# Optimization experiments

Hardware: AMD Instinct MI355X
Metric: run time of the kernel (lower is better)

The kernel has to match this reference:

```python
import jax, jax.numpy as jnp
import numpy as np

# dims
B, S, D, H, F = 4, 1024, 1024, 16, 4096
DH = D // H
THETA0 = 1.0   # base firing threshold of AdaptiveLIFNeuron
RHO = 0.9      # adaptation decay
EPS = 1e-5


def layer_norm(x, g, b):
    mu = jnp.mean(x, axis=-1, keepdims=True)
    var = jnp.mean((x - mu) ** 2, axis=-1, keepdims=True)
    return (x - mu) * jax.lax.rsqrt(var + EPS) * g + b


def spike(u):
    # Heaviside forward, sigmoid surrogate gradient (straight-through)
    sg = jax.nn.sigmoid(4.0 * u)
    hard = (u > 0).astype(u.dtype)
    return sg + jax.lax.stop_gradient(hard - sg)


def setup_inputs() -> dict:
    key = jax.random.key(0)
    ks = jax.random.split(key, 8)
    std = 0.02
    w = lambda k, shape: jax.random.normal(k, shape, jnp.float32) * std
    return {
        "x": jax.random.normal(ks[0], (B, S, D), jnp.float32),
        "Wq": w(ks[1], (D, D)), "bq": jnp.zeros((D,), jnp.float32),
        "Wk": w(ks[2], (D, D)), "bk": jnp.zeros((D,), jnp.float32),
        "Wv": w(ks[3], (D, D)), "bv": jnp.zeros((D,), jnp.float32),
        "Wo": w(ks[4], (D, D)), "bo": jnp.zeros((D,), jnp.float32),
        "g1": jnp.ones((D,), jnp.float32), "b1": jnp.zeros((D,), jnp.float32),
        "W1": w(ks[5], (D, F)), "bf1": jnp.zeros((F,), jnp.float32),
        "W2": w(ks[6], (F, D)), "bf2": jnp.zeros((D,), jnp.float32),
        "g2": jnp.ones((D,), jnp.float32), "b2": jnp.zeros((D,), jnp.float32),
        "decay": jnp.full((F,), 0.8, jnp.float32),  # per-feature membrane leak
        "beta": jnp.full((F,), 0.1, jnp.float32),   # per-feature threshold adaptation
    }


def reference(x, Wq, bq, Wk, bk, Wv, bv, Wo, bo, g1, b1, W1, bf1, W2, bf2, g2, b2, decay, beta):
    # --- causal multi-head self-attention (DSALayer) ---
    q = (x @ Wq + bq).reshape(B, S, H, DH)
    k = (x @ Wk + bk).reshape(B, S, H, DH)
    v = (x @ Wv + bv).reshape(B, S, H, DH)
    scores = jnp.einsum("bqhd,bkhd->bhqk", q, k) / np.sqrt(DH).astype(np.float32)
    causal = jnp.tril(jnp.ones((S, S), bool))
    scores = jnp.where(causal, scores, jnp.asarray(-1e9, scores.dtype))
    p = jax.nn.softmax(scores, axis=-1)
    attn = jnp.einsum("bhqk,bkhd->bqhd", p, v).reshape(B, S, D) @ Wo + bo
    h = layer_norm(x + attn, g1, b1)

    # --- feed-forward with per-timestep adaptive LIF recurrence ---
    ff = h @ W1 + bf1                      # [B, S, F]

    def step(carry, xt):
        vm, a = carry                      # membrane potential, adaptation
        vm = decay * vm + xt
        u = vm - (THETA0 + a)
        s = spike(u)
        vm = vm * (1.0 - s)                # hard reset on spike
        a = RHO * a + beta * s
        return (vm, a), s

    init = (jnp.zeros((B, F), x.dtype), jnp.zeros((B, F), x.dtype))
    _, spikes = jax.lax.scan(step, init, jnp.swapaxes(ff, 0, 1))  # scan over time
    spikes = jnp.swapaxes(spikes, 0, 1)    # [B, S, F]

    ff_out = spikes @ W2 + bf2
    return layer_norm(h + ff_out, g2, b2)
```

## Files before the change

kernel.cpp:

```cpp
#include <hip/hip_runtime.h>
#include <hip/hip_bf16.h>
#include <stdint.h>

#define Bsz 4
#define Ssz 1024
#define Dsz 1024
#define Hsz 16
#define Fsz 4096

typedef __hip_bfloat16 bf16;
typedef __attribute__((ext_vector_type(8))) short bf16x8;
typedef __attribute__((ext_vector_type(4))) float f32x4;

typedef __attribute__((address_space(1))) const void gvoid_t;
typedef __attribute__((address_space(3))) void svoid_t;

__device__ __forceinline__ void gload16(const bf16* g, bf16* l) {
    __builtin_amdgcn_global_load_lds((gvoid_t*)g, (svoid_t*)l, 16, 0, 0);
}

__global__ __launch_bounds__(256) void split_k(const float* __restrict__ src,
                                               bf16* __restrict__ hi,
                                               bf16* __restrict__ lo) {
    const int i = (blockIdx.x * 256 + threadIdx.x) * 4;
    const float4 v = *(const float4*)(src + i);
    float vv[4] = {v.x, v.y, v.z, v.w};
    #pragma unroll
    for (int u = 0; u < 4; ++u) {
        const bf16 h = __float2bfloat16(vv[u]);
        hi[i + u] = h;
        lo[i + u] = __float2bfloat16(vv[u] - __bfloat162float(h));
    }
}

__global__ __launch_bounds__(256) void transpose_split4_k(const float* __restrict__ Wq,
                                                          const float* __restrict__ Wk,
                                                          const float* __restrict__ Wv,
                                                          const float* __restrict__ Wo,
                                                          bf16* __restrict__ qkv_hi,
                                                          bf16* __restrict__ qkv_lo,
                                                          bf16* __restrict__ wo_hi,
                                                          bf16* __restrict__ wo_lo) {
    __shared__ float tile[32][33];
    const int z = blockIdx.z;
    const float* in = (z == 0) ? Wq : (z == 1) ? Wk : (z == 2) ? Wv : Wo;
    const size_t WP = (size_t)Dsz * Dsz;
    bf16* hiT = (z < 3) ? qkv_hi + (size_t)z * WP : wo_hi;
    bf16* loT = (z < 3) ? qkv_lo + (size_t)z * WP : wo_lo;
    const int bx = blockIdx.x * 32, by = blockIdx.y * 32;
    const int tx = threadIdx.x, ty = threadIdx.y;
    #pragma unroll
    for (int i = 0; i < 32; i += 8)
        tile[ty + i][tx] = in[(size_t)(by + ty + i) * Dsz + bx + tx];
    __syncthreads();
    #pragma unroll
    for (int i = 0; i < 32; i += 8) {
        const float v = tile[tx][ty + i];
        const bf16 h = __float2bfloat16(v);
        const size_t o = (size_t)(bx + ty + i) * Dsz + by + tx;
        hiT[o] = h;
        loT[o] = __float2bfloat16(v - __bfloat162float(h));
    }
}

__global__ __launch_bounds__(256) void transpose_split_k(const float* __restrict__ in,
                                                         bf16* __restrict__ hiT,
                                                         bf16* __restrict__ loT,
                                                         int R, int C) {
    __shared__ float tile[32][33];
    const int bx = blockIdx.x * 32, by = blockIdx.y * 32;
    const int tx = threadIdx.x, ty = threadIdx.y;
    #pragma unroll
    for (int i = 0; i < 32; i += 8)
        tile[ty + i][tx] = in[(size_t)(by + ty + i) * C + bx + tx];
    __syncthreads();
    #pragma unroll
    for (int i = 0; i < 32; i += 8) {
        const float v = tile[tx][ty + i];
        const bf16 h = __float2bfloat16(v);
        const size_t o = (size_t)(bx + ty + i) * R + by + tx;
        hiT[o] = h;
        loT[o] = __float2bfloat16(v - __bfloat162float(h));
    }
}

__global__ __launch_bounds__(256) void transpose_cast_k(const float* __restrict__ in,
                                                        bf16* __restrict__ outT,
                                                        int R, int C) {
    __shared__ float tile[32][33];
    const int bx = blockIdx.x * 32, by = blockIdx.y * 32;
    const int tx = threadIdx.x, ty = threadIdx.y;
    #pragma unroll
    for (int i = 0; i < 32; i += 8)
        tile[ty + i][tx] = in[(size_t)(by + ty + i) * C + bx + tx];
    __syncthreads();
    #pragma unroll
    for (int i = 0; i < 32; i += 8)
        outT[(size_t)(bx + ty + i) * R + by + tx] = __float2bfloat16(tile[tx][ty + i]);
}

__global__ __launch_bounds__(256) void gemm3_bt(const bf16* __restrict__ Ah,
                                                const bf16* __restrict__ Al,
                                                const bf16* __restrict__ Bh,
                                                const bf16* __restrict__ Bl,
                                                const float* __restrict__ bias,
                                                float* __restrict__ Cf,
                                                int M, int N, int K) {
    __shared__ alignas(16) bf16 Ash[128 * 32];
    __shared__ alignas(16) bf16 Asl[128 * 32];
    __shared__ alignas(16) bf16 Bsh[128 * 32];
    __shared__ alignas(16) bf16 Bsl[128 * 32];
    const int t = threadIdx.x;
    const int lane = t & 63, wv = t >> 6;
    const int mw = wv >> 1, nw = wv & 1;
    const int m0 = blockIdx.y * 128, n0 = blockIdx.x * 128;
    const int z = blockIdx.z, nz = gridDim.z;
    const int Ks = K / nz, koff = z * Ks;
    const int r16 = lane & 15, q8 = (lane >> 4) * 8;
    const int arow = t >> 2, acol = (t & 3) * 8;

    const bf16* gAh = Ah + (size_t)(m0 + arow) * K + koff + acol;
    const bf16* gAl = Al + (size_t)(m0 + arow) * K + koff + acol;
    const bf16* gBh = Bh + (size_t)(n0 + arow) * K + koff + acol;
    const bf16* gBl = Bl + (size_t)(n0 + arow) * K + koff + acol;
    const size_t rK64 = (size_t)64 * K;
    bf16* lAh = Ash + wv * 512;
    bf16* lAl = Asl + wv * 512;
    bf16* lBh = Bsh + wv * 512;
    bf16* lBl = Bsl + wv * 512;

    f32x4 acc[4][4] = {};

    for (int k0 = 0; k0 < Ks; k0 += 32) {
        __syncthreads();
        gload16(gAh + k0, lAh);  gload16(gAh + k0 + rK64, lAh + 2048);
        gload16(gAl + k0, lAl);  gload16(gAl + k0 + rK64, lAl + 2048);
        gload16(gBh + k0, lBh);  gload16(gBh + k0 + rK64, lBh + 2048);
        gload16(gBl + k0, lBl);  gload16(gBl + k0 + rK64, lBl + 2048);
        __syncthreads();

        bf16x8 ah[4], al[4], bh[4], bl[4];
        #pragma unroll
        for (int rt = 0; rt < 4; ++rt) {
            const int ro = (64 * mw + 16 * rt + r16) * 32 + q8;
            ah[rt] = *(const bf16x8*)(Ash + ro);
            al[rt] = *(const bf16x8*)(Asl + ro);
        }
        #pragma unroll
        for (int ct = 0; ct < 4; ++ct) {
            const int co = (64 * nw + 16 * ct + r16) * 32 + q8;
            bh[ct] = *(const bf16x8*)(Bsh + co);
            bl[ct] = *(const bf16x8*)(Bsl + co);
        }
        #pragma unroll
        for (int rt = 0; rt < 4; ++rt)
            #pragma unroll
            for (int ct = 0; ct < 4; ++ct) {
                acc[rt][ct] = __builtin_amdgcn_mfma_f32_16x16x32_bf16(ah[rt], bh[ct], acc[rt][ct], 0, 0, 0);
                acc[rt][ct] = __builtin_amdgcn_mfma_f32_16x16x32_bf16(ah[rt], bl[ct], acc[rt][ct], 0, 0, 0);
                acc[rt][ct] = __builtin_amdgcn_mfma_f32_16x16x32_bf16(al[rt], bh[ct], acc[rt][ct], 0, 0, 0);
            }
    }

    float* Cz = Cf + (size_t)z * M * N;
    const int rowi = (lane >> 4) * 4;
    const int coli = lane & 15;
    #pragma unroll
    for (int ct = 0; ct < 4; ++ct) {
        const int col = n0 + 64 * nw + 16 * ct + coli;
        const float bv = (z == 0) ? bias[col] : 0.f;
        #pragma unroll
        for (int rt = 0; rt < 4; ++rt) {
            const int rowb = m0 + 64 * mw + 16 * rt + rowi;
            #pragma unroll
            for (int r = 0; r < 4; ++r)
                Cz[(size_t)(rowb + r) * N + col] = acc[rt][ct][r] + bv;
        }
    }
}

__global__ __launch_bounds__(256) void gemm3_qkv(const bf16* __restrict__ Ah,
                                                 const bf16* __restrict__ Al,
                                                 const bf16* __restrict__ Bh,
                                                 const bf16* __restrict__ Bl,
                                                 const float* __restrict__ bias,
                                                 bf16* __restrict__ qhi, bf16* __restrict__ qlo,
                                                 bf16* __restrict__ khi, bf16* __restrict__ klo,
                                                 bf16* __restrict__ vthi, bf16* __restrict__ vtlo) {
    const int K = Dsz;
    __shared__ alignas(16) bf16 Ash[128 * 32];
    __shared__ alignas(16) bf16 Asl[128 * 32];
    __shared__ alignas(16) bf16 Bsh[128 * 32];
    __shared__ alignas(16) bf16 Bsl[128 * 32];
    const int t = threadIdx.x;
    const int lane = t & 63, wv = t >> 6;
    const int mw = wv >> 1, nw = wv & 1;
    const int m0 = blockIdx.y * 128, n0 = blockIdx.x * 128;
    const int r16 = lane & 15, q8 = (lane >> 4) * 8;
    const int arow = t >> 2, acol = (t & 3) * 8;

    const bf16* gAh = Ah + (size_t)(m0 + arow) * K + acol;
    const bf16* gAl = Al + (size_t)(m0 + arow) * K + acol;
    const bf16* gBh = Bh + (size_t)(n0 + arow) * K + acol;
    const bf16* gBl = Bl + (size_t)(n0 + arow) * K + acol;
    const size_t rK64 = (size_t)64 * K;
    bf16* lAh = Ash + wv * 512;
    bf16* lAl = Asl + wv * 512;
    bf16* lBh = Bsh + wv * 512;
    bf16* lBl = Bsl + wv * 512;

    f32x4 acc[4][4] = {};

    for (int k0 = 0; k0 < K; k0 += 32) {
        __syncthreads();
        gload16(gAh + k0, lAh);  gload16(gAh + k0 + rK64, lAh + 2048);
        gload16(gAl + k0, lAl);  gload16(gAl + k0 + rK64, lAl + 2048);
        gload16(gBh + k0, lBh);  gload16(gBh + k0 + rK64, lBh + 2048);
        gload16(gBl + k0, lBl);  gload16(gBl + k0 + rK64, lBl + 2048);
        __syncthreads();

        bf16x8 ah[4], al[4], bh[4], bl[4];
        #pragma unroll
        for (int rt = 0; rt < 4; ++rt) {
            const int ro = (64 * mw + 16 * rt + r16) * 32 + q8;
            ah[rt] = *(const bf16x8*)(Ash + ro);
            al[rt] = *(const bf16x8*)(Asl + ro);
        }
        #pragma unroll
        for (int ct = 0; ct < 4; ++ct) {
            const int co = (64 * nw + 16 * ct + r16) * 32 + q8;
            bh[ct] = *(const bf16x8*)(Bsh + co);
            bl[ct] = *(const bf16x8*)(Bsl + co);
        }
        #pragma unroll
        for (int rt = 0; rt < 4; ++rt)
            #pragma unroll
            for (int ct = 0; ct < 4; ++ct) {
                acc[rt][ct] = __builtin_amdgcn_mfma_f32_16x16x32_bf16(ah[rt], bh[ct], acc[rt][ct], 0, 0, 0);
                acc[rt][ct] = __builtin_amdgcn_mfma_f32_16x16x32_bf16(ah[rt], bl[ct], acc[rt][ct], 0, 0, 0);
                acc[rt][ct] = __builtin_amdgcn_mfma_f32_16x16x32_bf16(al[rt], bh[ct], acc[rt][ct], 0, 0, 0);
            }
    }

    const int rowi = (lane >> 4) * 4;
    const int coli = lane & 15;
    if (n0 < 2048) {
        const float scale = (n0 < 1024) ? 0.125f : 1.0f;
        bf16* hip_ = (n0 < 1024) ? qhi : khi;
        bf16* lop_ = (n0 < 1024) ? qlo : klo;
        const int cbase = (n0 < 1024) ? n0 : (n0 - 1024);
        #pragma unroll
        for (int ct = 0; ct < 4; ++ct) {
            const int col = cbase + 64 * nw + 16 * ct + coli;
            const float bv = bias[n0 + 64 * nw + 16 * ct + coli];
            #pragma unroll
            for (int rt = 0; rt < 4; ++rt) {
                const int rowb = m0 + 64 * mw + 16 * rt + rowi;
                #pragma unroll
                for (int r = 0; r < 4; ++r) {
                    const float val = (acc[rt][ct][r] + bv) * scale;
                    const bf16 h = __float2bfloat16(val);
                    const size_t off = (size_t)(rowb + r) * Dsz + col;
                    hip_[off] = h;
                    lop_[off] = __float2bfloat16(val - __bfloat162float(h));
                }
            }
        }
    } else {
        #pragma unroll
        for (int ct = 0; ct < 4; ++ct) {
            const int col = n0 + 64 * nw + 16 * ct + coli;
            const float bv = bias[col];
            const int c2 = col - 2048;
            #pragma unroll
            for (int rt = 0; rt < 4; ++rt) {
                const int rowb = m0 + 64 * mw + 16 * rt + rowi;
                const int b = rowb >> 10, s = rowb & 1023;
                bf16 hv[4], lv[4];
                #pragma unroll
                for (int r = 0; r < 4; ++r) {
                    const float val = acc[rt][ct][r] + bv;
                    hv[r] = __float2bfloat16(val);
                    lv[r] = __float2bfloat16(val - __bfloat162float(hv[r]));
                }
                const size_t vo = (size_t)b * (16 * 64 * 1024) + (size_t)c2 * 1024 + s;
                *(uint2*)&vthi[vo] = *(const uint2*)hv;
                *(uint2*)&vtlo[vo] = *(const uint2*)lv;
            }
        }
    }
}

__global__ __launch_bounds__(256) void gemm1_bt(const bf16* __restrict__ A,
                                                const bf16* __restrict__ Bt,
                                                const float* __restrict__ bias,
                                                float* __restrict__ Cf,
                                                int M, int N, int K) {
    __shared__ alignas(16) bf16 As[128 * 32];
    __shared__ alignas(16) bf16 Bs[128 * 32];
    const int t = threadIdx.x;
    const int lane = t & 63, wv = t >> 6;
    const int mw = wv >> 1, nw = wv & 1;
    const int m0 = blockIdx.y * 128, n0 = blockIdx.x * 128;
    const int z = blockIdx.z, nz = gridDim.z;
    const int Ks = K / nz, koff = z * Ks;
    const int r16 = lane & 15, q8 = (lane >> 4) * 8;
    const int arow = t >> 2, acol = (t & 3) * 8;

    const bf16* gA = A + (size_t)(m0 + arow) * K + koff + acol;
    const bf16* gB = Bt + (size_t)(n0 + arow) * K + koff + acol;
    const size_t rK64 = (size_t)64 * K;
    bf16* lA = As + wv * 512;
    bf16* lB = Bs + wv * 512;

    f32x4 acc[4][4] = {};

    for (int k0 = 0; k0 < Ks; k0 += 32) {
        __syncthreads();
        gload16(gA + k0, lA);  gload16(gA + k0 + rK64, lA + 2048);
        gload16(gB + k0, lB);  gload16(gB + k0 + rK64, lB + 2048);
        __syncthreads();

        bf16x8 af[4], bf_[4];
        #pragma unroll
        for (int rt = 0; rt < 4; ++rt)
            af[rt] = *(const bf16x8*)(As + (64 * mw + 16 * rt + r16) * 32 + q8);
        #pragma unroll
        for (int ct = 0; ct < 4; ++ct)
            bf_[ct] = *(const bf16x8*)(Bs + (64 * nw + 16 * ct + r16) * 32 + q8);
        #pragma unroll
        for (int rt = 0; rt < 4; ++rt)
            #pragma unroll
            for (int ct = 0; ct < 4; ++ct)
                acc[rt][ct] = __builtin_amdgcn_mfma_f32_16x16x32_bf16(
                    af[rt], bf_[ct], acc[rt][ct], 0, 0, 0);
    }

    float* Cz = Cf + (size_t)z * M * N;
    const int rowi = (lane >> 4) * 4;
    const int coli = lane & 15;
    #pragma unroll
    for (int ct = 0; ct < 4; ++ct) {
        const int col = n0 + 64 * nw + 16 * ct + coli;
        const float bv = (z == 0) ? bias[col] : 0.f;
        #pragma unroll
        for (int rt = 0; rt < 4; ++rt) {
            const int rowb = m0 + 64 * mw + 16 * rt + rowi;
            #pragma unroll
            for (int r = 0; r < 4; ++r)
                Cz[(size_t)(rowb + r) * N + col] = acc[rt][ct][r] + bv;
        }
    }
}

__global__ __launch_bounds__(256) void attn_mfma_k(const bf16* __restrict__ qhp,
                                                   const bf16* __restrict__ qlp,
                                                   const bf16* __restrict__ khp,
                                                   const bf16* __restrict__ klp,
                                                   const bf16* __restrict__ vhp,
                                                   const bf16* __restrict__ vlp,
                                                   bf16* __restrict__ ohi,
                                                   bf16* __restrict__ olo) {
    __shared__ alignas(16) float Pf[64 * 68];
    __shared__ alignas(16) bf16 Kh[64 * 72], Kl[64 * 72];
    __shared__ alignas(16) bf16 Vh[64 * 72], Vl[64 * 72];

    const int bh = blockIdx.y;
    const int b = bh >> 4, h = bh & 15;
    const int q0 = (gridDim.x - 1 - blockIdx.x) * 64;
    const int t = threadIdx.x, w = t >> 6, lane = t & 63;
    const int r16 = lane & 15, quad = lane >> 4;
    const int sr = t >> 2, sc = (t & 3) * 16;

    bf16x8 aQh[2], aQl[2];
    {
        const size_t qb = (size_t)(b * Ssz + q0 + 16 * w + r16) * Dsz + h * 64 + quad * 8;
        aQh[0] = *(const bf16x8*)(qhp + qb);
        aQh[1] = *(const bf16x8*)(qhp + qb + 32);
        aQl[0] = *(const bf16x8*)(qlp + qb);
        aQl[1] = *(const bf16x8*)(qlp + qb + 32);
    }

    f32x4 aco[4] = {};
    float lrun[4] = {0.f, 0.f, 0.f, 0.f};
    const int ntiles = q0 / 64 + 1;

    for (int kt = 0; kt < ntiles; ++kt) {
        __syncthreads();
        {
            const size_t g = (size_t)(b * Ssz + kt * 64 + sr) * Dsz + h * 64 + sc;
            *(uint4*)&Kh[sr * 72 + sc]     = *(const uint4*)(khp + g);
            *(uint4*)&Kh[sr * 72 + sc + 8] = *(const uint4*)(khp + g + 8);
            *(uint4*)&Kl[sr * 72 + sc]     = *(const uint4*)(klp + g);
            *(uint4*)&Kl[sr * 72 + sc + 8] = *(const uint4*)(klp + g + 8);
            const size_t gv = ((size_t)bh * 64 + sr) * Ssz + kt * 64 + sc;
            *(uint4*)&Vh[sr * 72 + sc]     = *(const uint4*)(vhp + gv);
            *(uint4*)&Vh[sr * 72 + sc + 8] = *(const uint4*)(vhp + gv + 8);
            *(uint4*)&Vl[sr * 72 + sc]     = *(const uint4*)(vlp + gv);
            *(uint4*)&Vl[sr * 72 + sc + 8] = *(const uint4*)(vlp + gv + 8);
        }
        __syncthreads();

        #pragma unroll
        for (int nt = 0; nt < 4; ++nt) {
            f32x4 s = {};
            #pragma unroll
            for (int ks = 0; ks < 2; ++ks) {
                const bf16x8 bKh = *(const bf16x8*)&Kh[(16 * nt + r16) * 72 + ks * 32 + quad * 8];
                const bf16x8 bKl = *(const bf16x8*)&Kl[(16 * nt + r16) * 72 + ks * 32 + quad * 8];
                s = __builtin_amdgcn_mfma_f32_16x16x32_bf16(aQh[ks], bKh, s, 0, 0, 0);
                s = __builtin_amdgcn_mfma_f32_16x16x32_bf16(aQh[ks], bKl, s, 0, 0, 0);
                s = __builtin_amdgcn_mfma_f32_16x16x32_bf16(aQl[ks], bKh, s, 0, 0, 0);
            }
            const int key = kt * 64 + nt * 16 + r16;
            #pragma unroll
            for (int r = 0; r < 4; ++r) {
                const int qrow = q0 + 16 * w + quad * 4 + r;
                const float p = (key <= qrow) ? __expf(s[r]) : 0.f;
                lrun[r] += p;
                Pf[(16 * w + quad * 4 + r) * 68 + nt * 16 + r16] = p;
            }
        }

        bf16x8 aPh[2], aPl[2];
        #pragma unroll
        for (int ks = 0; ks < 2; ++ks) {
            const float4 pa = *(const float4*)&Pf[(16 * w + r16) * 68 + ks * 32 + quad * 8];
            const float4 pb = *(const float4*)&Pf[(16 * w + r16) * 68 + ks * 32 + quad * 8 + 4];
            const float pv[8] = {pa.x, pa.y, pa.z, pa.w, pb.x, pb.y, pb.z, pb.w};
            bf16 hv[8], lv[8];
            #pragma unroll
            for (int j = 0; j < 8; ++j) {
                hv[j] = __float2bfloat16(pv[j]);
                lv[j] = __float2bfloat16(pv[j] - __bfloat162float(hv[j]));
            }
            aPh[ks] = *(const bf16x8*)hv;
            aPl[ks] = *(const bf16x8*)lv;
        }

        #pragma unroll
        for (int nt = 0; nt < 4; ++nt) {
            #pragma unroll
            for (int ks = 0; ks < 2; ++ks) {
                const bf16x8 bVh = *(const bf16x8*)&Vh[(16 * nt + r16) * 72 + ks * 32 + quad * 8];
                const bf16x8 bVl = *(const bf16x8*)&Vl[(16 * nt + r16) * 72 + ks * 32 + quad * 8];
                aco[nt] = __builtin_amdgcn_mfma_f32_16x16x32_bf16(aPh[ks], bVh, aco[nt], 0, 0, 0);
                aco[nt] = __builtin_amdgcn_mfma_f32_16x16x32_bf16(aPh[ks], bVl, aco[nt], 0, 0, 0);
                aco[nt] = __builtin_amdgcn_mfma_f32_16x16x32_bf16(aPl[ks], bVh, aco[nt], 0, 0, 0);
            }
        }
    }

    #pragma unroll
    for (int r = 0; r < 4; ++r) {
        float l = lrun[r];
        l += __shfl_xor(l, 1); l += __shfl_xor(l, 2);
        l += __shfl_xor(l, 4); l += __shfl_xor(l, 8);
        lrun[r] = l;
    }
    #pragma unroll
    for (int nt = 0; nt < 4; ++nt)
        #pragma unroll
        for (int r = 0; r < 4; ++r) {
            const size_t off = (size_t)(b * Ssz + q0 + 16 * w + quad * 4 + r) * Dsz
                               + h * 64 + nt * 16 + r16;
            const float val = aco[nt][r] / lrun[r];
            const bf16 hh = __float2bfloat16(val);
            ohi[off] = hh;
            olo[off] = __float2bfloat16(val - __bfloat162float(hh));
        }
}

__global__ __launch_bounds__(64) void scan_k(const float* __restrict__ ff,
                                             const float* __restrict__ decay,
                                             const float* __restrict__ beta,
                                             bf16* __restrict__ spikes) {
    const int idx = blockIdx.x * 64 + threadIdx.x;
    const int b = idx >> 12;
    const int f = idx & (Fsz - 1);
    const float dec = decay[f];
    const float bet = beta[f];
    const float* src = ff + (size_t)b * Ssz * Fsz + f;
    bf16* dst = spikes + (size_t)b * Ssz * Fsz + f;
    float vm = 0.f, a = 0.f;
    float buf[64];
    #pragma unroll
    for (int u = 0; u < 64; ++u) buf[u] = src[(size_t)u * Fsz];
    for (int gg = 0; gg < 16; ++gg) {
        #pragma unroll
        for (int sub = 0; sub < 4; ++sub) {
            const int g = gg * 4 + sub;
            #pragma unroll
            for (int u = 0; u < 16; ++u) {
                vm = dec * vm + buf[sub * 16 + u];
                const float uu = vm - (1.f + a);
                const float sp = (uu > 0.f) ? 1.f : 0.f;
                vm = (uu > 0.f) ? 0.f : vm;
                a = 0.9f * a + bet * sp;
                dst[(size_t)(g * 16 + u) * Fsz] = __float2bfloat16(sp);
            }
            if (g + 4 < 64) {
                #pragma unroll
                for (int u = 0; u < 16; ++u)
                    buf[sub * 16 + u] = src[(size_t)((g + 4) * 16 + u) * Fsz];
            }
        }
    }
}

__device__ __forceinline__ float block_sum(float val, float* ls, int t) {
    #pragma unroll
    for (int mm = 32; mm >= 1; mm >>= 1) val += __shfl_xor(val, mm);
    if ((t & 63) == 0) ls[t >> 6] = val;
    __syncthreads();
    const float r = ls[0] + ls[1] + ls[2] + ls[3];
    __syncthreads();
    return r;
}

__global__ __launch_bounds__(256) void ln1_k(const float* __restrict__ x,
                                             const float* __restrict__ ap0,
                                             const float* __restrict__ ap1,
                                             const float* __restrict__ g,
                                             const float* __restrict__ bb,
                                             bf16* __restrict__ h_hi,
                                             bf16* __restrict__ h_lo) {
    __shared__ float ls[4];
    const int row = blockIdx.x;
    const int t = threadIdx.x;
    const size_t base = (size_t)row * Dsz;
    float vv[4];
    #pragma unroll
    for (int i = 0; i < 4; ++i) {
        const int c = t + i * 256;
        vv[i] = x[base + c] + (ap0[base + c] + ap1[base + c]);
    }
    float s = vv[0] + vv[1] + vv[2] + vv[3];
    s = block_sum(s, ls, t);
    const float mu = s * (1.f / 1024.f);
    float qs = 0.f;
    #pragma unroll
    for (int i = 0; i < 4; ++i) { const float d = vv[i] - mu; qs += d * d; }
    qs = block_sum(qs, ls, t);
    const float rs = rsqrtf(qs * (1.f / 1024.f) + 1e-5f);
    #pragma unroll
    for (int i = 0; i < 4; ++i) {
        const int c = t + i * 256;
        const float o = (vv[i] - mu) * rs * g[c] + bb[c];
        const bf16 hi = __float2bfloat16(o);
        h_hi[base + c] = hi;
        h_lo[base + c] = __float2bfloat16(o - __bfloat162float(hi));
    }
}

__global__ __launch_bounds__(256) void ln2_k(const bf16* __restrict__ h_hi,
                                             const bf16* __restrict__ h_lo,
                                             const float* __restrict__ fo0,
                                             const float* __restrict__ fo1,
                                             const float* __restrict__ g,
                                             const float* __restrict__ bb,
                                             float* __restrict__ out) {
    __shared__ float ls[4];
    const int row = blockIdx.x;
    const int t = threadIdx.x;
    const size_t base = (size_t)row * Dsz;
    float vv[4];
    #pragma unroll
    for (int i = 0; i < 4; ++i) {
        const int c = t + i * 256;
        const float h = __bfloat162float(h_hi[base + c]) + __bfloat162float(h_lo[base + c]);
        vv[i] = h + (fo0[base + c] + fo1[base + c]);
    }
    float s = vv[0] + vv[1] + vv[2] + vv[3];
    s = block_sum(s, ls, t);
    const float mu = s * (1.f / 1024.f);
    float qs = 0.f;
    #pragma unroll
    for (int i = 0; i < 4; ++i) { const float d = vv[i] - mu; qs += d * d; }
    qs = block_sum(qs, ls, t);
    const float rs = rsqrtf(qs * (1.f / 1024.f) + 1e-5f);
    #pragma unroll
    for (int i = 0; i < 4; ++i) {
        const int c = t + i * 256;
        out[base + c] = (vv[i] - mu) * rs * g[c] + bb[c];
    }
}

extern "C" void kernel_launch(void* const* d_in, const int* in_sizes, int n_in,
                              void* d_out, int out_size, void* d_ws, size_t ws_size,
                              hipStream_t stream) {
    const float* x    = (const float*)d_in[0];
    const float* Wq   = (const float*)d_in[1];
    const float* bq   = (const float*)d_in[2];
    const float* Wk   = (const float*)d_in[3];
    const float* bk   = (const float*)d_in[4];
    const float* Wv   = (const float*)d_in[5];
    const float* bv   = (const float*)d_in[6];
    const float* Wo   = (const float*)d_in[7];
    const float* bo   = (const float*)d_in[8];
    const float* g1   = (const float*)d_in[9];
    const float* b1   = (const float*)d_in[10];
    const float* W1   = (const float*)d_in[11];
    const float* bf1  = (const float*)d_in[12];
    const float* W2   = (const float*)d_in[13];
    const float* bf2  = (const float*)d_in[14];
    const float* g2   = (const float*)d_in[15];
    const float* b2   = (const float*)d_in[16];
    const float* dec  = (const float*)d_in[17];
    const float* beta = (const float*)d_in[18];

    const size_t BSD = (size_t)Bsz * Ssz * Dsz;
    const size_t BSF = (size_t)Bsz * Ssz * Fsz;

    char* ws = (char*)d_ws;
    char* A3 = ws;
    char* A1 = A3 + BSF * 4;
    char* A2 = A1 + BSF * 2;
    char* A4 = A2 + (size_t)Dsz * Fsz * 2 * 2;
    float* bqkv = (float*)(A4 + BSD * 4);

    bf16* qhi   = (bf16*)(A3);
    bf16* qlo   = (bf16*)(A3 + BSD * 2);
    bf16* khi   = (bf16*)(A3 + BSD * 4);
    bf16* klo   = (bf16*)(A3 + BSD * 6);
    float* attnp = (float*)(A3);
    float* ffb   = (float*)(A3);
    float* ffout = (float*)(A3);

    bf16* xhi    = (bf16*)(A1);
    bf16* xlo    = (bf16*)(A1 + BSD * 2);
    bf16* athi   = (bf16*)(A1);
    bf16* atlo   = (bf16*)(A1 + BSD * 2);
    bf16* spikes = (bf16*)(A1);

    const size_t WP = (size_t)Dsz * Dsz;
    bf16* Wqkv_hi = (bf16*)(A2);
    bf16* Wqkv_lo = (bf16*)(A2 + WP * 3 * 2);
    bf16* WoThi   = (bf16*)(A2 + WP * 6 * 2);
    bf16* WoTlo   = (bf16*)(A2 + WP * 7 * 2);
    bf16* W1Thi   = (bf16*)(A2);
    bf16* W1Tlo   = (bf16*)(A2 + (size_t)Dsz * Fsz * 2);
    bf16* W2T     = (bf16*)(A2);

    bf16* vthi  = (bf16*)(A4);
    bf16* vtlo  = (bf16*)(A4 + BSD * 2);
    bf16* h_hi  = (bf16*)(A4);
    bf16* h_lo  = (bf16*)(A4 + BSD * 2);

    (void)ws_size; (void)in_sizes; (void)n_in; (void)out_size;

    const dim3 tb(32, 8);
    const int MBS = Bsz * Ssz;

    split_k<<<BSD / 1024, 256, 0, stream>>>(x, xhi, xlo);
    transpose_split4_k<<<dim3(32, 32, 4), tb, 0, stream>>>(
        Wq, Wk, Wv, Wo, Wqkv_hi, Wqkv_lo, WoThi, WoTlo);
    hipMemcpyAsync(bqkv,        (const void*)bq, Dsz * 4, hipMemcpyDeviceToDevice, stream);
    hipMemcpyAsync(bqkv + 1024, (const void*)bk, Dsz * 4, hipMemcpyDeviceToDevice, stream);
    hipMemcpyAsync(bqkv + 2048, (const void*)bv, Dsz * 4, hipMemcpyDeviceToDevice, stream);

    gemm3_qkv<<<dim3(3072 / 128, MBS / 128), 256, 0, stream>>>(
        xhi, xlo, Wqkv_hi, Wqkv_lo, bqkv, qhi, qlo, khi, klo, vthi, vtlo);

    attn_mfma_k<<<dim3(Ssz / 64, Bsz * Hsz), 256, 0, stream>>>(
        qhi, qlo, khi, klo, vthi, vtlo, athi, atlo);

    gemm3_bt<<<dim3(Dsz / 128, MBS / 128, 2), 256, 0, stream>>>(
        athi, atlo, WoThi, WoTlo, bo, attnp, MBS, Dsz, Dsz);
    ln1_k<<<MBS, 256, 0, stream>>>(x, attnp, attnp + (size_t)MBS * Dsz,
                                   g1, b1, h_hi, h_lo);

    transpose_split_k<<<dim3(Fsz / 32, Dsz / 32), tb, 0, stream>>>(W1, W1Thi, W1Tlo, Dsz, Fsz);
    gemm3_bt<<<dim3(Fsz / 128, MBS / 128, 1), 256, 0, stream>>>(
        h_hi, h_lo, W1Thi, W1Tlo, bf1, ffb, MBS, Fsz, Dsz);

    scan_k<<<Bsz * Fsz / 64, 64, 0, stream>>>(ffb, dec, beta, spikes);

    transpose_cast_k<<<dim3(Dsz / 32, Fsz / 32), tb, 0, stream>>>(W2, W2T, Fsz, Dsz);
    gemm1_bt<<<dim3(Dsz / 128, MBS / 128, 2), 256, 0, stream>>>(
        spikes, W2T, bf2, ffout, MBS, Dsz, Fsz);

    ln2_k<<<MBS, 256, 0, stream>>>(h_hi, h_lo, ffout, ffout + (size_t)MBS * Dsz,
                                   g2, b2, (float*)d_out);
}
```

Baseline: 624.0 us.

## Restructure causal attention to 128-query blocks reading K/V directly, fuse bias copies

The attention kernel now gives each block 128 queries, with each wave owning 32 rows, and reads K/V fragments straight from global memory instead of staging them in LDS behind barriers. Each K/V fragment is reused across two query sub-tiles, and every wave runs only as many key tiles as its own causal range needs. The grid is reordered so the batch-head index is the fast dimension. Separately, the three bias hipMemcpyAsync calls are folded into split_k to remove launch overhead. The trade-off is more redundant global and L2 traffic, since each of the four waves loads K/V independently, plus higher register pressure and fewer, larger blocks.

After: 599.8 us. -3.9%, faster.

```diff
diff --git a/kernel.cpp b/kernel.cpp
--- a/kernel.cpp
+++ b/kernel.cpp
@@ -21,7 +21,11 @@
 
 __global__ __launch_bounds__(256) void split_k(const float* __restrict__ src,
                                                bf16* __restrict__ hi,
-                                               bf16* __restrict__ lo) {
+                                               bf16* __restrict__ lo,
+                                               const float* __restrict__ bq,
+                                               const float* __restrict__ bk,
+                                               const float* __restrict__ bv,
+                                               float* __restrict__ bqkv) {
     const int i = (blockIdx.x * 256 + threadIdx.x) * 4;
     const float4 v = *(const float4*)(src + i);
     float vv[4] = {v.x, v.y, v.z, v.w};
@@ -30,6 +34,11 @@
         const bf16 h = __float2bfloat16(vv[u]);
         hi[i + u] = h;
         lo[i + u] = __float2bfloat16(vv[u] - __bfloat162float(h));
+    }
+    if (blockIdx.x < 3) {
+        const float* bsrc = (blockIdx.x == 0) ? bq : (blockIdx.x == 1) ? bk : bv;
+        const int j = threadIdx.x * 4;
+        *(float4*)(bqkv + blockIdx.x * 1024 + j) = *(const float4*)(bsrc + j);
     }
 }
 
@@ -361,114 +370,117 @@
                                                    const bf16* __restrict__ vlp,
                                                    bf16* __restrict__ ohi,
                                                    bf16* __restrict__ olo) {
-    __shared__ alignas(16) float Pf[64 * 68];
-    __shared__ alignas(16) bf16 Kh[64 * 72], Kl[64 * 72];
-    __shared__ alignas(16) bf16 Vh[64 * 72], Vl[64 * 72];
-
-    const int bh = blockIdx.y;
+    __shared__ alignas(16) float Pf[128 * 68];
+
+    const int bh = blockIdx.x;
     const int b = bh >> 4, h = bh & 15;
-    const int q0 = (gridDim.x - 1 - blockIdx.x) * 64;
+    const int q0b = blockIdx.y * 128;
     const int t = threadIdx.x, w = t >> 6, lane = t & 63;
     const int r16 = lane & 15, quad = lane >> 4;
-    const int sr = t >> 2, sc = (t & 3) * 16;
-
-    bf16x8 aQh[2], aQl[2];
-    {
-        const size_t qb = (size_t)(b * Ssz + q0 + 16 * w + r16) * Dsz + h * 64 + quad * 8;
-        aQh[0] = *(const bf16x8*)(qhp + qb);
-        aQh[1] = *(const bf16x8*)(qhp + qb + 32);
-        aQl[0] = *(const bf16x8*)(qlp + qb);
-        aQl[1] = *(const bf16x8*)(qlp + qb + 32);
-    }
-
-    f32x4 aco[4] = {};
-    float lrun[4] = {0.f, 0.f, 0.f, 0.f};
-    const int ntiles = q0 / 64 + 1;
+    const int qw = q0b + 32 * w;
+
+    bf16x8 aQh[2][2], aQl[2][2];
+    #pragma unroll
+    for (int mt = 0; mt < 2; ++mt) {
+        const size_t qb = (size_t)(b * Ssz + qw + 16 * mt + r16) * Dsz + h * 64 + quad * 8;
+        aQh[mt][0] = *(const bf16x8*)(qhp + qb);
+        aQh[mt][1] = *(const bf16x8*)(qhp + qb + 32);
+        aQl[mt][0] = *(const bf16x8*)(qlp + qb);
+        aQl[mt][1] = *(const bf16x8*)(qlp + qb + 32);
+    }
+
+    f32x4 aco[2][4] = {};
+    float lrun[2][4] = {};
+    const int ntiles = (qw + 31) / 64 + 1;
 
     for (int kt = 0; kt < ntiles; ++kt) {
-        __syncthreads();
-        {
-            const size_t g = (size_t)(b * Ssz + kt * 64 + sr) * Dsz + h * 64 + sc;
-            *(uint4*)&Kh[sr * 72 + sc]     = *(const uint4*)(khp + g);
-            *(uint4*)&Kh[sr * 72 + sc + 8] = *(const uint4*)(khp + g + 8);
-            *(uint4*)&Kl[sr * 72 + sc]     = *(const uint4*)(klp + g);
-            *(uint4*)&Kl[sr * 72 + sc + 8] = *(const uint4*)(klp + g + 8);
-            const size_t gv = ((size_t)bh * 64 + sr) * Ssz + kt * 64 + sc;
-            *(uint4*)&Vh[sr * 72 + sc]     = *(const uint4*)(vhp + gv);
-            *(uint4*)&Vh[sr * 72 + sc + 8] = *(const uint4*)(vhp + gv + 8);
-            *(uint4*)&Vl[sr * 72 + sc]     = *(const uint4*)(vlp + gv);
-            *(uint4*)&Vl[sr * 72 + sc + 8] = *(const uint4*)(vlp + gv + 8);
-        }
-        __syncthreads();
-
         #pragma unroll
         for (int nt = 0; nt < 4; ++nt) {
-            f32x4 s = {};
+            const size_t kb = (size_t)(b * Ssz + kt * 64 + nt * 16 + r16) * Dsz + h * 64 + quad * 8;
+            const bf16x8 bKh0 = *(const bf16x8*)(khp + kb);
+            const bf16x8 bKh1 = *(const bf16x8*)(khp + kb + 32);
+            const bf16x8 bKl0 = *(const bf16x8*)(klp + kb);
+            const bf16x8 bKl1 = *(const bf16x8*)(klp + kb + 32);
+            const int key = kt * 64 + nt * 16 + r16;
+            #pragma unroll
+            for (int mt = 0; mt < 2; ++mt) {
+                f32x4 s = {};
+                s = __builtin_amdgcn_mfma_f32_16x16x32_bf16(aQh[mt][0], bKh0, s, 0, 0, 0);
+                s = __builtin_amdgcn_mfma_f32_16x16x32_bf16(aQh[mt][0], bKl0, s, 0, 0, 0);
+                s = __builtin_amdgcn_mfma_f32_16x16x32_bf16(aQl[mt][0], bKh0, s, 0, 0, 0);
+                s = __builtin_amdgcn_mfma_f32_16x16x32_bf16(aQh[mt][1], bKh1, s, 0, 0, 0);
+                s = __builtin_amdgcn_mfma_f32_16x16x32_bf16(aQh[mt][1], bKl1, s, 0, 0, 0);
+                s = __builtin_amdgcn_mfma_f32_16x16x32_bf16(aQl[mt][1], bKh1, s, 0, 0, 0);
+                #pragma unroll
+                for (int r = 0; r < 4; ++r) {
+                    const int qrow = qw + 16 * mt + quad * 4 + r;
+                    const float p = (key <= qrow) ? __expf(s[r]) : 0.f;
+                    lrun[mt][r] += p;
+                    Pf[(32 * w + 16 * mt + quad * 4 + r) * 68 + nt * 16 + r16] = p;
+                }
+            }
+        }
+
+        bf16x8 aPh[2][2], aPl[2][2];
+        #pragma unroll
+        for (int mt = 0; mt < 2; ++mt)
             #pragma unroll
             for (int ks = 0; ks < 2; ++ks) {
-                const bf16x8 bKh = *(const bf16x8*)&Kh[(16 * nt + r16) * 72 + ks * 32 + quad * 8];
-                const bf16x8 bKl = *(const bf16x8*)&Kl[(16 * nt + r16) * 72 + ks * 32 + quad * 8];
-                s = __builtin_amdgcn_mfma_f32_16x16x32_bf16(aQh[ks], bKh, s, 0, 0, 0);
-                s = __builtin_amdgcn_mfma_f32_16x16x32_bf16(aQh[ks], bKl, s, 0, 0, 0);
-                s = __builtin_amdgcn_mfma_f32_16x16x32_bf16(aQl[ks], bKh, s, 0, 0, 0);
-            }
-            const int key = kt * 64 + nt * 16 + r16;
+                const float* pr = &Pf[(32 * w + 16 * mt + r16) * 68 + ks * 32 + quad * 8];
+                const float4 pa = *(const float4*)pr;
+                const float4 pb = *(const float4*)(pr + 4);
+                const float pv[8] = {pa.x, pa.y, pa.z, pa.w, pb.x, pb.y, pb.z, pb.w};
+                bf16 hv[8], lv[8];
+                #pragma unroll
+                for (int j = 0; j < 8; ++j) {
+                    hv[j] = __float2bfloat16(pv[j]);
+                    lv[j] = __float2bfloat16(pv[j] - __bfloat162float(hv[j]));
+                }
+                aPh[mt][ks] = *(const bf16x8*)hv;
+                aPl[mt][ks] = *(const bf16x8*)lv;
+            }
+
+        #pragma unroll
+        for (int nt = 0; nt < 4; ++nt) {
+            const size_t vb = ((size_t)bh * 64 + nt * 16 + r16) * Ssz + kt * 64 + quad * 8;
+            const bf16x8 bVh0 = *(const bf16x8*)(vhp + vb);
+            const bf16x8 bVh1 = *(const bf16x8*)(vhp + vb + 32);
+            const bf16x8 bVl0 = *(const bf16x8*)(vlp + vb);
+            const bf16x8 bVl1 = *(const bf16x8*)(vlp + vb + 32);
+            #pragma unroll
+            for (int mt = 0; mt < 2; ++mt) {
+                aco[mt][nt] = __builtin_amdgcn_mfma_f32_16x16x32_bf16(aPh[mt][0], bVh0, aco[mt][nt], 0, 0, 0);
+                aco[mt][nt] = __builtin_amdgcn_mfma_f32_16x16x32_bf16(aPh[mt][0], bVl0, aco[mt][nt], 0, 0, 0);
+                aco[mt][nt] = __builtin_amdgcn_mfma_f32_16x16x32_bf16(aPl[mt][0], bVh0, aco[mt][nt], 0, 0, 0);
+                aco[mt][nt] = __builtin_amdgcn_mfma_f32_16x16x32_bf16(aPh[mt][1], bVh1, aco[mt][nt], 0, 0, 0);
+                aco[mt][nt] = __builtin_amdgcn_mfma_f32_16x16x32_bf16(aPh[mt][1], bVl1, aco[mt][nt], 0, 0, 0);
+                aco[mt][nt] = __builtin_amdgcn_mfma_f32_16x16x32_bf16(aPl[mt][1], bVh1, aco[mt][nt], 0, 0, 0);
+            }
+        }
+    }
+
+    #pragma unroll
+    for (int mt = 0; mt < 2; ++mt)
+        #pragma unroll
+        for (int r = 0; r < 4; ++r) {
+            float l = lrun[mt][r];
+            l += __shfl_xor(l, 1); l += __shfl_xor(l, 2);
+            l += __shfl_xor(l, 4); l += __shfl_xor(l, 8);
+            lrun[mt][r] = l;
+        }
+    #pragma unroll
+    for (int mt = 0; mt < 2; ++mt)
+        #pragma unroll
+        for (int nt = 0; nt < 4; ++nt)
             #pragma unroll
             for (int r = 0; r < 4; ++r) {
-                const int qrow = q0 + 16 * w + quad * 4 + r;
-                const float p = (key <= qrow) ? __expf(s[r]) : 0.f;
-                lrun[r] += p;
-                Pf[(16 * w + quad * 4 + r) * 68 + nt * 16 + r16] = p;
-            }
-        }
-
-        bf16x8 aPh[2], aPl[2];
-        #pragma unroll
-        for (int ks = 0; ks < 2; ++ks) {
-            const float4 pa = *(const float4*)&Pf[(16 * w + r16) * 68 + ks * 32 + quad * 8];
-            const float4 pb = *(const float4*)&Pf[(16 * w + r16) * 68 + ks * 32 + quad * 8 + 4];
-            const float pv[8] = {pa.x, pa.y, pa.z, pa.w, pb.x, pb.y, pb.z, pb.w};
-            bf16 hv[8], lv[8];
-            #pragma unroll
-            for (int j = 0; j < 8; ++j) {
-                hv[j] = __float2bfloat16(pv[j]);
-                lv[j] = __float2bfloat16(pv[j] - __bfloat162float(hv[j]));
-            }
-            aPh[ks] = *(const bf16x8*)hv;
-            aPl[ks] = *(const bf16x8*)lv;
-        }
-
-        #pragma unroll
-        for (int nt = 0; nt < 4; ++nt) {
-            #pragma unroll
-            for (int ks = 0; ks < 2; ++ks) {
-                const bf16x8 bVh = *(const bf16x8*)&Vh[(16 * nt + r16) * 72 + ks * 32 + quad * 8];
-                const bf16x8 bVl = *(const bf16x8*)&Vl[(16 * nt + r16) * 72 + ks * 32 + quad * 8];
-                aco[nt] = __builtin_amdgcn_mfma_f32_16x16x32_bf16(aPh[ks], bVh, aco[nt], 0, 0, 0);
-                aco[nt] = __builtin_amdgcn_mfma_f32_16x16x32_bf16(aPh[ks], bVl, aco[nt], 0, 0, 0);
-                aco[nt] = __builtin_amdgcn_mfma_f32_16x16x32_bf16(aPl[ks], bVh, aco[nt], 0, 0, 0);
-            }
-        }
-    }
-
-    #pragma unroll
-    for (int r = 0; r < 4; ++r) {
-        float l = lrun[r];
-        l += __shfl_xor(l, 1); l += __shfl_xor(l, 2);
-        l += __shfl_xor(l, 4); l += __shfl_xor(l, 8);
-        lrun[r] = l;
-    }
-    #pragma unroll
-    for (int nt = 0; nt < 4; ++nt)
-        #pragma unroll
-        for (int r = 0; r < 4; ++r) {
-            const size_t off = (size_t)(b * Ssz + q0 + 16 * w + quad * 4 + r) * Dsz
-                               + h * 64 + nt * 16 + r16;
-            const float val = aco[nt][r] / lrun[r];
-            const bf16 hh = __float2bfloat16(val);
-            ohi[off] = hh;
-            olo[off] = __float2bfloat16(val - __bfloat162float(hh));
-        }
+                const size_t off = (size_t)(b * Ssz + qw + 16 * mt + quad * 4 + r) * Dsz
+                                   + h * 64 + nt * 16 + r16;
+                const float val = aco[mt][nt][r] / lrun[mt][r];
+                const bf16 hh = __float2bfloat16(val);
+                ohi[off] = hh;
+                olo[off] = __float2bfloat16(val - __bfloat162float(hh));
+            }
 }
 
 __global__ __launch_bounds__(64) void scan_k(const float* __restrict__ ff,
@@ -652,17 +664,14 @@
     const dim3 tb(32, 8);
     const int MBS = Bsz * Ssz;
 
-    split_k<<<BSD / 1024, 256, 0, stream>>>(x, xhi, xlo);
+    split_k<<<BSD / 1024, 256, 0, stream>>>(x, xhi, xlo, bq, bk, bv, bqkv);
     transpose_split4_k<<<dim3(32, 32, 4), tb, 0, stream>>>(
         Wq, Wk, Wv, Wo, Wqkv_hi, Wqkv_lo, WoThi, WoTlo);
-    hipMemcpyAsync(bqkv,        (const void*)bq, Dsz * 4, hipMemcpyDeviceToDevice, stream);
-    hipMemcpyAsync(bqkv + 1024, (const void*)bk, Dsz * 4, hipMemcpyDeviceToDevice, stream);
-    hipMemcpyAsync(bqkv + 2048, (const void*)bv, Dsz * 4, hipMemcpyDeviceToDevice, stream);
 
     gemm3_qkv<<<dim3(3072 / 128, MBS / 128), 256, 0, stream>>>(
         xhi, xlo, Wqkv_hi, Wqkv_lo, bqkv, qhi, qlo, khi, klo, vthi, vtlo);
 
-    attn_mfma_k<<<dim3(Ssz / 64, Bsz * Hsz), 256, 0, stream>>>(
+    attn_mfma_k<<<dim3(Bsz * Hsz, Ssz / 128), 256, 0, stream>>>(
         qhi, qlo, khi, klo, vthi, vtlo, athi, atlo);
 
     gemm3_bt<<<dim3(Dsz / 128, MBS / 128, 2), 256, 0, stream>>>(
```
